# Kernel tuning notes

Hardware: AMD Instinct MI355X
Metric: run time of the kernel (lower is better)

The kernel has to match this reference:

```python
import jax, jax.numpy as jnp
import numpy as np

N = 100000        # nodes
E = 1600000       # edges (before self loops)
F_IN = 14         # Mutagenicity num_node_features
H = 64            # hidden_channels
C = 2             # Mutagenicity num_classes
G = 512           # graphs in batch
NEG_SLOPE = 0.2   # GATConv default leaky slope for attention logits


def setup_inputs() -> dict:
    key = jax.random.key(0)
    ks = jax.random.split(key, 40)
    inp = {
        "x": jax.random.normal(ks[0], (N, F_IN), jnp.float32),
        "edge_index": jax.random.randint(ks[1], (2, E), 0, N, dtype=jnp.int64),
        "batch": jnp.sort(jax.random.randint(ks[2], (N,), 0, G, dtype=jnp.int64)),
    }
    dims = [F_IN, H, H, H, H]
    ki = 3
    for l in range(5):
        fin = dims[l]
        s = 1.0 / np.sqrt(fin)
        inp[f"W{l}"] = jax.random.uniform(ks[ki], (fin, H), jnp.float32, -s, s); ki += 1
        inp[f"a_src{l}"] = jax.random.uniform(ks[ki], (H,), jnp.float32, -0.3, 0.3); ki += 1
        inp[f"a_dst{l}"] = jax.random.uniform(ks[ki], (H,), jnp.float32, -0.3, 0.3); ki += 1
        inp[f"b{l}"] = jnp.zeros((H,), jnp.float32)
    s = 1.0 / np.sqrt(H)
    inp["lin_W"] = jax.random.uniform(ks[ki], (H, C), jnp.float32, -s, s); ki += 1
    inp["lin_b"] = jnp.zeros((C,), jnp.float32)
    return inp


def _gat_layer(x, src, dst, W, a_s, a_d, b):
    # GATConv (heads=1): h = x W; e_ij = LeakyReLU(a_s.h_j + a_d.h_i);
    # alpha = softmax over incoming edges of node i; out_i = sum_j alpha_ij h_j + b
    h = x @ W                                   # [N, H]
    logit_s = h @ a_s                           # [N]
    logit_d = h @ a_d                           # [N]
    e = jax.nn.leaky_relu(logit_s[src] + logit_d[dst], NEG_SLOPE)  # [Etot]
    m = jax.ops.segment_max(e, dst, num_segments=N)
    m = jnp.where(jnp.isfinite(m), m, 0.0)      # empty segments -> 0 (none after self loops)
    ex = jnp.exp(e - m[dst])
    den = jax.ops.segment_sum(ex, dst, num_segments=N)
    alpha = ex / den[dst]                       # self loops guarantee den > 0
    out = jax.ops.segment_sum(alpha[:, None] * h[src], dst, num_segments=N)
    return out + b


def reference(x, edge_index, batch,
              W0, a_src0, a_dst0, b0,
              W1, a_src1, a_dst1, b1,
              W2, a_src2, a_dst2, b2,
              W3, a_src3, a_dst3, b3,
              W4, a_src4, a_dst4, b4,
              lin_W, lin_b):
    # add self loops once (GATConv default add_self_loops=True)
    loop = jnp.arange(N, dtype=edge_index.dtype)
    src = jnp.concatenate([edge_index[0], loop])
    dst = jnp.concatenate([edge_index[1], loop])

    h = x
    layers = [(W0, a_src0, a_dst0, b0), (W1, a_src1, a_dst1, b1),
              (W2, a_src2, a_dst2, b2), (W3, a_src3, a_dst3, b3),
              (W4, a_src4, a_dst4, b4)]
    for (W, a_s, a_d, b) in layers:
        h = jax.nn.elu(_gat_layer(h, src, dst, W, a_s, a_d, b))

    # global max pool over graphs
    g = jax.ops.segment_max(h, batch, num_segments=G)   # [G, H]
    g = jnp.where(jnp.isfinite(g), g, 0.0)
    return g @ lin_W + lin_b                             # [G, C]
```

## Files before the change

### kernel.cpp

```cpp
#include <hip/hip_runtime.h>
#include <hip/hip_fp16.h>
#include <math.h>

#define N_NODES 100000
#define H_DIM 64
#define G_GRAPHS 512
#define NEG_SLOPE 0.2f

#define BSHIFT 9
#define NBKT ((N_NODES + (1 << BSHIFT) - 1) >> BSHIFT)
#define CHUNK_E 4096

#define DEG_CAP 32

#define PK_SRC(v)  ((v) & 0x1FFFF)
#define PK_LD(v)   ((v) >> 17)

#if defined(__has_builtin)
#if __has_builtin(__builtin_amdgcn_fdot2)
#define HAS_FDOT2 1
#endif
#endif
#ifndef HAS_FDOT2
#define HAS_FDOT2 0
#endif

#if HAS_FDOT2
typedef _Float16 h2_t __attribute__((ext_vector_type(2)));
__device__ __forceinline__ h2_t as_h2(unsigned u) {
    h2_t r; __builtin_memcpy(&r, &u, 4); return r;
}
#endif


__global__ __launch_bounds__(256) void bucket_hist_kernel(const int* __restrict__ dst,
                                                          int* __restrict__ bcount, int E) {
    __shared__ int lh[NBKT];
    int t = threadIdx.x;
    for (int i = t; i < NBKT; i += 256) lh[i] = 0;
    __syncthreads();
    int base = blockIdx.x * CHUNK_E;
#pragma unroll
    for (int k = 0; k < 16; ++k) {
        int e = base + k * 256 + t;
        if (e < E) atomicAdd(&lh[dst[e] >> BSHIFT], 1);
    }
    __syncthreads();
    for (int i = t; i < NBKT; i += 256) {
        int c = lh[i];
        if (c) atomicAdd(&bcount[i], c);
    }
}

__global__ __launch_bounds__(256) void bucket_scan_kernel(const int* __restrict__ bcount,
                                                          int* __restrict__ bbase,
                                                          int* __restrict__ bfill,
                                                          int* __restrict__ off, int n) {
    __shared__ int sm[256];
    int t = threadIdx.x;
    sm[t] = (t < NBKT) ? bcount[t] : 0;
    __syncthreads();
    for (int d = 1; d < 256; d <<= 1) {
        int v = (t >= d) ? sm[t - d] : 0;
        __syncthreads();
        sm[t] += v;
        __syncthreads();
    }
    if (t < NBKT) {
        int ex = (t == 0) ? 0 : sm[t - 1];
        bbase[t] = ex;
        bfill[t] = ex;
    }
    if (t == 0) {
        bbase[NBKT] = sm[255];
        off[n] = sm[255];
    }
}

__global__ __launch_bounds__(256) void partition_kernel(const int* __restrict__ src,
                                                        const int* __restrict__ dst,
                                                        int* __restrict__ bfill,
                                                        int* __restrict__ ebuck, int E) {
    __shared__ int lh[NBKT];
    __shared__ int lbase[NBKT];
    int t = threadIdx.x;
    int base = blockIdx.x * CHUNK_E;
    for (int i = t; i < NBKT; i += 256) lh[i] = 0;
    __syncthreads();

    int pk[16], bk[16];
#pragma unroll
    for (int k = 0; k < 16; ++k) {
        int e = base + k * 256 + t;
        if (e < E) {
            int s = src[e];
            int d = dst[e];
            bk[k] = d >> BSHIFT;
            pk[k] = s | ((d & ((1 << BSHIFT) - 1)) << 17);
            atomicAdd(&lh[bk[k]], 1);
        } else {
            bk[k] = -1;
        }
    }
    __syncthreads();
    for (int i = t; i < NBKT; i += 256) {
        int c = lh[i];
        lbase[i] = c ? atomicAdd(&bfill[i], c) : 0;
        lh[i] = 0;
    }
    __syncthreads();
#pragma unroll
    for (int k = 0; k < 16; ++k) {
        if (bk[k] >= 0) {
            int r = atomicAdd(&lh[bk[k]], 1);
            ebuck[lbase[bk[k]] + r] = pk[k];
        }
    }
}

__global__ __launch_bounds__(256) void bucket_csr_kernel(const int* __restrict__ ebuck,
                                                         const int* __restrict__ bbase,
                                                         int* __restrict__ off,
                                                         int* __restrict__ esrc, int n) {
    __shared__ int cnt[512];
    __shared__ int loff[512];
    __shared__ int sm[256];
    int b = blockIdx.x;
    int t = threadIdx.x;
    int ebeg = bbase[b];
    int eend = bbase[b + 1];
    int nbeg = b << BSHIFT;
    int nloc = n - nbeg; if (nloc > 512) nloc = 512;

    cnt[t] = 0; cnt[t + 256] = 0;
    __syncthreads();
    for (int e = ebeg + t; e < eend; e += 256) {
        atomicAdd(&cnt[PK_LD(ebuck[e])], 1);
    }
    __syncthreads();
    int c0 = cnt[2 * t], c1 = cnt[2 * t + 1];
    sm[t] = c0 + c1;
    __syncthreads();
    for (int d = 1; d < 256; d <<= 1) {
        int v = (t >= d) ? sm[t - d] : 0;
        __syncthreads();
        sm[t] += v;
        __syncthreads();
    }
    int basep = (t == 0) ? 0 : sm[t - 1];
    loff[2 * t] = basep;
    loff[2 * t + 1] = basep + c0;
    cnt[2 * t] = 0; cnt[2 * t + 1] = 0;
    __syncthreads();
    for (int i = t; i < nloc; i += 256) off[nbeg + i] = ebeg + loff[i];
    for (int e = ebeg + t; e < eend; e += 256) {
        int v = ebuck[e];
        int d = PK_LD(v);
        int r = atomicAdd(&cnt[d], 1);
        esrc[ebeg + loff[d] + r] = PK_SRC(v);
    }
}

template <int FIN, int FINP, int XSTR>
__global__ __launch_bounds__(256) void gemm_tile_kernel(
        const float* __restrict__ act, const float* __restrict__ W,
        const float* __restrict__ a_s, const float* __restrict__ a_d,
        __half* __restrict__ h16g,
        float* __restrict__ ls, float* __restrict__ ld,
        int n) {
    __shared__ float sx[128 * XSTR];
    __shared__ float sw[FINP * 64];
    int t = threadIdx.x;
    int tb = blockIdx.x * 128;
    int nrow = n - tb; if (nrow > 128) nrow = 128;

    {
        const float4* Wv = (const float4*)W;
        float4* swv = (float4*)sw;
        for (int i = t; i < FINP * 16; i += 256) {
            int k = i >> 4;
            swv[i] = (k < FIN) ? Wv[i] : make_float4(0.0f, 0.0f, 0.0f, 0.0f);
        }
    }
    {
        int c = t & 15;
        for (int r = t >> 4; r < 128; r += 16) {
            float v = 0.0f;
            if (r < nrow && c < FIN) v = act[(size_t)(tb + r) * FIN + c];
            sx[r * XSTR + c] = v;
        }
    }
    __syncthreads();

    int f4 = t & 15;
    int ng = t >> 4;

    float4 acc[8];
#pragma unroll
    for (int i = 0; i < 8; ++i) acc[i] = make_float4(0.0f, 0.0f, 0.0f, 0.0f);

    for (int k4 = 0; k4 < FINP; k4 += 4) {
        float4 w0 = *(const float4*)(sw + (k4 + 0) * 64 + f4 * 4);
        float4 w1 = *(const float4*)(sw + (k4 + 1) * 64 + f4 * 4);
        float4 w2 = *(const float4*)(sw + (k4 + 2) * 64 + f4 * 4);
        float4 w3 = *(const float4*)(sw + (k4 + 3) * 64 + f4 * 4);
#pragma unroll
        for (int i = 0; i < 8; ++i) {
            float4 xv = *(const float4*)(sx + (ng + 16 * i) * XSTR + k4);
            acc[i].x = fmaf(xv.x, w0.x, acc[i].x);
            acc[i].y = fmaf(xv.x, w0.y, acc[i].y);
            acc[i].z = fmaf(xv.x, w0.z, acc[i].z);
            acc[i].w = fmaf(xv.x, w0.w, acc[i].w);
            acc[i].x = fmaf(xv.y, w1.x, acc[i].x);
            acc[i].y = fmaf(xv.y, w1.y, acc[i].y);
            acc[i].z = fmaf(xv.y, w1.z, acc[i].z);
            acc[i].w = fmaf(xv.y, w1.w, acc[i].w);
            acc[i].x = fmaf(xv.z, w2.x, acc[i].x);
            acc[i].y = fmaf(xv.z, w2.y, acc[i].y);
            acc[i].z = fmaf(xv.z, w2.z, acc[i].z);
            acc[i].w = fmaf(xv.z, w2.w, acc[i].w);
            acc[i].x = fmaf(xv.w, w3.x, acc[i].x);
            acc[i].y = fmaf(xv.w, w3.y, acc[i].y);
            acc[i].z = fmaf(xv.w, w3.z, acc[i].z);
            acc[i].w = fmaf(xv.w, w3.w, acc[i].w);
        }
    }

    float4 as4 = *(const float4*)(a_s + f4 * 4);
    float4 ad4 = *(const float4*)(a_d + f4 * 4);
#pragma unroll
    for (int i = 0; i < 8; ++i) {
        int r = ng + 16 * i;
        if (r < nrow) {
            int node = tb + r;
            __half2 plo = __floats2half2_rn(acc[i].x, acc[i].y);
            __half2 phi = __floats2half2_rn(acc[i].z, acc[i].w);
            uint2 pk;
            pk.x = *reinterpret_cast<unsigned*>(&plo);
            pk.y = *reinterpret_cast<unsigned*>(&phi);
            *reinterpret_cast<uint2*>(h16g + (size_t)node * 64 + f4 * 4) = pk;
            float vs = acc[i].x * as4.x + acc[i].y * as4.y +
                       acc[i].z * as4.z + acc[i].w * as4.w;
            float vd = acc[i].x * ad4.x + acc[i].y * ad4.y +
                       acc[i].z * ad4.z + acc[i].w * ad4.w;
            vs += __shfl_xor(vs, 1, 64); vd += __shfl_xor(vd, 1, 64);
            vs += __shfl_xor(vs, 2, 64); vd += __shfl_xor(vd, 2, 64);
            vs += __shfl_xor(vs, 4, 64); vd += __shfl_xor(vd, 4, 64);
            vs += __shfl_xor(vs, 8, 64); vd += __shfl_xor(vd, 8, 64);
            if (f4 == 0) { ls[node] = vs; ld[node] = vd; }
        }
    }
}

__global__ __launch_bounds__(256) void gat_gemm_kernel(
        const __half* __restrict__ h16_in, const float* __restrict__ ls_in,
        const float* __restrict__ ld_in, const int* __restrict__ off,
        const int* __restrict__ esrc, const float* __restrict__ bias,
        const float* __restrict__ Wn, const float* __restrict__ asn,
        const float* __restrict__ adn,
        __half* __restrict__ h16_out, float* __restrict__ ls_out,
        float* __restrict__ ld_out, int n) {
#if HAS_FDOT2
    __shared__ unsigned sw2[32 * 64];
#else
    __shared__ float sw[64 * 64];
#endif
    __shared__ int2 smq[16 * DEG_CAP];
    int t = threadIdx.x;
#if HAS_FDOT2
    for (int i = t; i < 32 * 64; i += 256) {
        int k2 = i >> 6, f = i & 63;
        float w0 = Wn[(2 * k2) * 64 + f];
        float w1 = Wn[(2 * k2 + 1) * 64 + f];
        __half2 wp = __floats2half2_rn(w0, w1);
        sw2[i] = *reinterpret_cast<unsigned*>(&wp);
    }
#else
    {
        const float4* Wv = (const float4*)Wn;
        float4* swv = (float4*)sw;
        for (int i = t; i < 64 * 16; i += 256) swv[i] = Wv[i];
    }
#endif
    __syncthreads();

    int fl = t & 15;
    int g = t >> 4;
    int node = blockIdx.x * 16 + g;
    if (node >= n) return;
    int2* sq = smq + g * DEG_CAP;
    int fl4 = fl * 4;
    int sk4 = 4 * g;

    int jb = off[node];
    int je = off[node + 1];
    int deg = je - jb;
    int degc = (deg < DEG_CAP) ? deg : DEG_CAP;
    float ldv = ld_in[node];
    float lself = ls_in[node];

    float mm = lself;
    for (int c = fl; c < degc; c += 16) {
        int s = esrc[jb + c];
        float v = ls_in[s];
        sq[(c + sk4) & (DEG_CAP - 1)] = make_int2(s, __float_as_int(v));
        mm = fmaxf(mm, v);
    }
    for (int c = degc + fl; c < deg; c += 16) {
        mm = fmaxf(mm, ls_in[esrc[jb + c]]);
    }
    mm = fmaxf(mm, __shfl_xor(mm, 8, 64));
    mm = fmaxf(mm, __shfl_xor(mm, 4, 64));
    mm = fmaxf(mm, __shfl_xor(mm, 2, 64));
    mm = fmaxf(mm, __shfl_xor(mm, 1, 64));
    float mraw = mm + ldv;
    float m = (mraw >= 0.0f) ? mraw : NEG_SLOPE * mraw;

    float denl = 0.0f;
    for (int c = fl; c < degc; c += 16) {
        int ci = (c + sk4) & (DEG_CAP - 1);
        float e = __int_as_float(sq[ci].y) + ldv;
        e = (e >= 0.0f) ? e : NEG_SLOPE * e;
        float p = __expf(e - m);
        sq[ci].y = __float_as_int(p);
        denl += p;
    }
    int degc4 = (degc + 3) & ~3;
    if (fl < degc4 - degc) sq[(degc + fl + sk4) & (DEG_CAP - 1)] = make_int2(node, 0);

    denl += __shfl_xor(denl, 8, 64);
    denl += __shfl_xor(denl, 4, 64);
    denl += __shfl_xor(denl, 2, 64);
    denl += __shfl_xor(denl, 1, 64);

    uint2 qs = *reinterpret_cast<const uint2*>(h16_in + (size_t)node * 64 + fl4);
    float2 sa = __half22float2(*reinterpret_cast<__half2*>(&qs.x));
    float2 sb = __half22float2(*reinterpret_cast<__half2*>(&qs.y));

    float4 acc = make_float4(0.0f, 0.0f, 0.0f, 0.0f);
    for (int c = 0; c < degc4; c += 4) {
        int2 e0 = sq[(c + 0 + sk4) & (DEG_CAP - 1)];
        int2 e1 = sq[(c + 1 + sk4) & (DEG_CAP - 1)];
        int2 e2 = sq[(c + 2 + sk4) & (DEG_CAP - 1)];
        int2 e3 = sq[(c + 3 + sk4) & (DEG_CAP - 1)];
        uint2 q0 = *reinterpret_cast<const uint2*>(h16_in + (size_t)e0.x * 64 + fl4);
        uint2 q1 = *reinterpret_cast<const uint2*>(h16_in + (size_t)e1.x * 64 + fl4);
        uint2 q2 = *reinterpret_cast<const uint2*>(h16_in + (size_t)e2.x * 64 + fl4);
        uint2 q3 = *reinterpret_cast<const uint2*>(h16_in + (size_t)e3.x * 64 + fl4);
        float p0 = __int_as_float(e0.y), p1 = __int_as_float(e1.y);
        float p2 = __int_as_float(e2.y), p3 = __int_as_float(e3.y);
        float2 a0 = __half22float2(*reinterpret_cast<__half2*>(&q0.x));
        float2 b0 = __half22float2(*reinterpret_cast<__half2*>(&q0.y));
        float2 a1 = __half22float2(*reinterpret_cast<__half2*>(&q1.x));
        float2 b1 = __half22float2(*reinterpret_cast<__half2*>(&q1.y));
        float2 a2 = __half22float2(*reinterpret_cast<__half2*>(&q2.x));
        float2 b2 = __half22float2(*reinterpret_cast<__half2*>(&q2.y));
        float2 a3 = __half22float2(*reinterpret_cast<__half2*>(&q3.x));
        float2 b3 = __half22float2(*reinterpret_cast<__half2*>(&q3.y));
        acc.x = fmaf(p0, a0.x, acc.x); acc.y = fmaf(p0, a0.y, acc.y);
        acc.z = fmaf(p0, b0.x, acc.z); acc.w = fmaf(p0, b0.y, acc.w);
        acc.x = fmaf(p1, a1.x, acc.x); acc.y = fmaf(p1, a1.y, acc.y);
        acc.z = fmaf(p1, b1.x, acc.z); acc.w = fmaf(p1, b1.y, acc.w);
        acc.x = fmaf(p2, a2.x, acc.x); acc.y = fmaf(p2, a2.y, acc.y);
        acc.z = fmaf(p2, b2.x, acc.z); acc.w = fmaf(p2, b2.y, acc.w);
        acc.x = fmaf(p3, a3.x, acc.x); acc.y = fmaf(p3, a3.y, acc.y);
        acc.z = fmaf(p3, b3.x, acc.z); acc.w = fmaf(p3, b3.y, acc.w);
    }

    float den_of = 0.0f;
    for (int j = jb + DEG_CAP; j < je; ++j) {
        int s = esrc[j];
        float e = ls_in[s] + ldv;
        e = (e >= 0.0f) ? e : NEG_SLOPE * e;
        float p = __expf(e - m);
        den_of += p;
        uint2 qv = *reinterpret_cast<const uint2*>(h16_in + (size_t)s * 64 + fl4);
        float2 va = __half22float2(*reinterpret_cast<__half2*>(&qv.x));
        float2 vb = __half22float2(*reinterpret_cast<__half2*>(&qv.y));
        acc.x = fmaf(p, va.x, acc.x);
        acc.y = fmaf(p, va.y, acc.y);
        acc.z = fmaf(p, vb.x, acc.z);
        acc.w = fmaf(p, vb.y, acc.w);
    }

    float e0s = lself + ldv;
    e0s = (e0s >= 0.0f) ? e0s : NEG_SLOPE * e0s;
    float p0s = __expf(e0s - m);
    float den = denl + den_of + p0s;
    acc.x = fmaf(p0s, sa.x, acc.x);
    acc.y = fmaf(p0s, sa.y, acc.y);
    acc.z = fmaf(p0s, sb.x, acc.z);
    acc.w = fmaf(p0s, sb.y, acc.w);

    const float4 b4 = *(const float4*)(bias + fl4);
    float inv = 1.0f / den;
    float4 o;
    o.x = acc.x * inv + b4.x;
    o.y = acc.y * inv + b4.y;
    o.z = acc.z * inv + b4.z;
    o.w = acc.w * inv + b4.w;
    o.x = (o.x > 0.0f) ? o.x : expm1f(o.x);
    o.y = (o.y > 0.0f) ? o.y : expm1f(o.y);
    o.z = (o.z > 0.0f) ? o.z : expm1f(o.z);
    o.w = (o.w > 0.0f) ? o.w : expm1f(o.w);

    float4 ha = make_float4(0.0f, 0.0f, 0.0f, 0.0f);
#if HAS_FDOT2
    {
        __half2 plo = __floats2half2_rn(o.x, o.y);
        __half2 phi = __floats2half2_rn(o.z, o.w);
        uint2 pk;
        pk.x = *reinterpret_cast<unsigned*>(&plo);
        pk.y = *reinterpret_cast<unsigned*>(&phi);
        uint2* so16 = (uint2*)sq;
        so16[(fl + g) & 15] = pk;
#pragma unroll
        for (int kk = 0; kk < 16; ++kk) {
            uint2 ov = so16[(kk + g) & 15];
            h2_t o01 = as_h2(ov.x);
            h2_t o23 = as_h2(ov.y);
            const uint4 wA = *reinterpret_cast<const uint4*>(sw2 + (2 * kk) * 64 + fl4);
            const uint4 wB = *reinterpret_cast<const uint4*>(sw2 + (2 * kk + 1) * 64 + fl4);
            ha.x = __builtin_amdgcn_fdot2(o01, as_h2(wA.x), ha.x, false);
            ha.y = __builtin_amdgcn_fdot2(o01, as_h2(wA.y), ha.y, false);
            ha.z = __builtin_amdgcn_fdot2(o01, as_h2(wA.z), ha.z, false);
            ha.w = __builtin_amdgcn_fdot2(o01, as_h2(wA.w), ha.w, false);
            ha.x = __builtin_amdgcn_fdot2(o23, as_h2(wB.x), ha.x, false);
            ha.y = __builtin_amdgcn_fdot2(o23, as_h2(wB.y), ha.y, false);
            ha.z = __builtin_amdgcn_fdot2(o23, as_h2(wB.z), ha.z, false);
            ha.w = __builtin_amdgcn_fdot2(o23, as_h2(wB.w), ha.w, false);
        }
    }
#else
    {
        float4* so = (float4*)sq;
        so[(fl + g) & 15] = o;
#pragma unroll
        for (int kk = 0; kk < 16; ++kk) {
            float4 ov = so[(kk + g) & 15];
            const float4 w0 = *(const float4*)(sw + (4 * kk + 0) * 64 + fl4);
            const float4 w1 = *(const float4*)(sw + (4 * kk + 1) * 64 + fl4);
            const float4 w2 = *(const float4*)(sw + (4 * kk + 2) * 64 + fl4);
            const float4 w3 = *(const float4*)(sw + (4 * kk + 3) * 64 + fl4);
            ha.x = fmaf(ov.x, w0.x, ha.x); ha.y = fmaf(ov.x, w0.y, ha.y);
            ha.z = fmaf(ov.x, w0.z, ha.z); ha.w = fmaf(ov.x, w0.w, ha.w);
            ha.x = fmaf(ov.y, w1.x, ha.x); ha.y = fmaf(ov.y, w1.y, ha.y);
            ha.z = fmaf(ov.y, w1.z, ha.z); ha.w = fmaf(ov.y, w1.w, ha.w);
            ha.x = fmaf(ov.z, w2.x, ha.x); ha.y = fmaf(ov.z, w2.y, ha.y);
            ha.z = fmaf(ov.z, w2.z, ha.z); ha.w = fmaf(ov.z, w2.w, ha.w);
            ha.x = fmaf(ov.w, w3.x, ha.x); ha.y = fmaf(ov.w, w3.y, ha.y);
            ha.z = fmaf(ov.w, w3.z, ha.z); ha.w = fmaf(ov.w, w3.w, ha.w);
        }
    }
#endif

    {
        __half2 plo = __floats2half2_rn(ha.x, ha.y);
        __half2 phi = __floats2half2_rn(ha.z, ha.w);
        uint2 pk;
        pk.x = *reinterpret_cast<unsigned*>(&plo);
        pk.y = *reinterpret_cast<unsigned*>(&phi);
        *reinterpret_cast<uint2*>(h16_out + (size_t)node * 64 + fl4) = pk;
    }
    float4 as4 = *(const float4*)(asn + fl4);
    float4 ad4 = *(const float4*)(adn + fl4);
    float vs = ha.x * as4.x + ha.y * as4.y + ha.z * as4.z + ha.w * as4.w;
    float vd = ha.x * ad4.x + ha.y * ad4.y + ha.z * ad4.z + ha.w * ad4.w;
    vs += __shfl_xor(vs, 1, 64); vd += __shfl_xor(vd, 1, 64);
    vs += __shfl_xor(vs, 2, 64); vd += __shfl_xor(vd, 2, 64);
    vs += __shfl_xor(vs, 4, 64); vd += __shfl_xor(vd, 4, 64);
    vs += __shfl_xor(vs, 8, 64); vd += __shfl_xor(vd, 8, 64);
    if (fl == 0) { ls_out[node] = vs; ld_out[node] = vd; }
}

__device__ __forceinline__ unsigned enc_f32(float f) {
    unsigned b = __float_as_uint(f);
    return (b & 0x80000000u) ? ~b : (b | 0x80000000u);
}

__global__ __launch_bounds__(256) void gat_final_pool_kernel(
        const __half* __restrict__ h16_in,
        const float* __restrict__ ls_in,
        const float* __restrict__ ld_in, const int* __restrict__ off,
        const int* __restrict__ esrc, const float* __restrict__ bias,
        const int* __restrict__ batch, unsigned* __restrict__ genc, int n) {
    __shared__ int2 smq[16 * DEG_CAP];
    __shared__ float sbo[16 * 64];
    __shared__ int sbb[16];
    int t = threadIdx.x;
    int fl = t & 15;
    int g = t >> 4;
    int node = blockIdx.x * 16 + g;
    bool active = node < n;
    int2* sq = smq + g * DEG_CAP;
    int fl4 = fl * 4;
    int sk4 = 4 * g;

    if (active) {
        int jb = off[node];
        int je = off[node + 1];
        int deg = je - jb;
        int degc = (deg < DEG_CAP) ? deg : DEG_CAP;
        float ldv = ld_in[node];
        float lself = ls_in[node];

        float mm = lself;
        for (int c = fl; c < degc; c += 16) {
            int s = esrc[jb + c];
            float v = ls_in[s];
            sq[(c + sk4) & (DEG_CAP - 1)] = make_int2(s, __float_as_int(v));
            mm = fmaxf(mm, v);
        }
        for (int c = degc + fl; c < deg; c += 16) {
            mm = fmaxf(mm, ls_in[esrc[jb + c]]);
        }
        mm = fmaxf(mm, __shfl_xor(mm, 8, 64));
        mm = fmaxf(mm, __shfl_xor(mm, 4, 64));
        mm = fmaxf(mm, __shfl_xor(mm, 2, 64));
        mm = fmaxf(mm, __shfl_xor(mm, 1, 64));
        float mraw = mm + ldv;
        float m = (mraw >= 0.0f) ? mraw : NEG_SLOPE * mraw;

        float denl = 0.0f;
        for (int c = fl; c < degc; c += 16) {
            int ci = (c + sk4) & (DEG_CAP - 1);
            float e = __int_as_float(sq[ci].y) + ldv;
            e = (e >= 0.0f) ? e : NEG_SLOPE * e;
            float p = __expf(e - m);
            sq[ci].y = __float_as_int(p);
            denl += p;
        }
        int degc4 = (degc + 3) & ~3;
        if (fl < degc4 - degc) sq[(degc + fl + sk4) & (DEG_CAP - 1)] = make_int2(node, 0);

        denl += __shfl_xor(denl, 8, 64);
        denl += __shfl_xor(denl, 4, 64);
        denl += __shfl_xor(denl, 2, 64);
        denl += __shfl_xor(denl, 1, 64);

        uint2 qs = *reinterpret_cast<const uint2*>(h16_in + (size_t)node * 64 + fl4);
        float2 sa = __half22float2(*reinterpret_cast<__half2*>(&qs.x));
        float2 sb = __half22float2(*reinterpret_cast<__half2*>(&qs.y));

        float4 acc = make_float4(0.0f, 0.0f, 0.0f, 0.0f);
        for (int c = 0; c < degc4; c += 4) {
            int2 e0 = sq[(c + 0 + sk4) & (DEG_CAP - 1)];
            int2 e1 = sq[(c + 1 + sk4) & (DEG_CAP - 1)];
            int2 e2 = sq[(c + 2 + sk4) & (DEG_CAP - 1)];
            int2 e3 = sq[(c + 3 + sk4) & (DEG_CAP - 1)];
            uint2 q0 = *reinterpret_cast<const uint2*>(h16_in + (size_t)e0.x * 64 + fl4);
            uint2 q1 = *reinterpret_cast<const uint2*>(h16_in + (size_t)e1.x * 64 + fl4);
            uint2 q2 = *reinterpret_cast<const uint2*>(h16_in + (size_t)e2.x * 64 + fl4);
            uint2 q3 = *reinterpret_cast<const uint2*>(h16_in + (size_t)e3.x * 64 + fl4);
            float p0 = __int_as_float(e0.y), p1 = __int_as_float(e1.y);
            float p2 = __int_as_float(e2.y), p3 = __int_as_float(e3.y);
            float2 a0 = __half22float2(*reinterpret_cast<__half2*>(&q0.x));
            float2 b0 = __half22float2(*reinterpret_cast<__half2*>(&q0.y));
            float2 a1 = __half22float2(*reinterpret_cast<__half2*>(&q1.x));
            float2 b1 = __half22float2(*reinterpret_cast<__half2*>(&q1.y));
            float2 a2 = __half22float2(*reinterpret_cast<__half2*>(&q2.x));
            float2 b2 = __half22float2(*reinterpret_cast<__half2*>(&q2.y));
            float2 a3 = __half22float2(*reinterpret_cast<__half2*>(&q3.x));
            float2 b3 = __half22float2(*reinterpret_cast<__half2*>(&q3.y));
            acc.x = fmaf(p0, a0.x, acc.x); acc.y = fmaf(p0, a0.y, acc.y);
            acc.z = fmaf(p0, b0.x, acc.z); acc.w = fmaf(p0, b0.y, acc.w);
            acc.x = fmaf(p1, a1.x, acc.x); acc.y = fmaf(p1, a1.y, acc.y);
            acc.z = fmaf(p1, b1.x, acc.z); acc.w = fmaf(p1, b1.y, acc.w);
            acc.x = fmaf(p2, a2.x, acc.x); acc.y = fmaf(p2, a2.y, acc.y);
            acc.z = fmaf(p2, b2.x, acc.z); acc.w = fmaf(p2, b2.y, acc.w);
            acc.x = fmaf(p3, a3.x, acc.x); acc.y = fmaf(p3, a3.y, acc.y);
            acc.z = fmaf(p3, b3.x, acc.z); acc.w = fmaf(p3, b3.y, acc.w);
        }

        float den_of = 0.0f;
        for (int j = jb + DEG_CAP; j < je; ++j) {
            int s = esrc[j];
            float e = ls_in[s] + ldv;
            e = (e >= 0.0f) ? e : NEG_SLOPE * e;
            float p = __expf(e - m);
            den_of += p;
            uint2 qv = *reinterpret_cast<const uint2*>(h16_in + (size_t)s * 64 + fl4);
            float2 va = __half22float2(*reinterpret_cast<__half2*>(&qv.x));
            float2 vb = __half22float2(*reinterpret_cast<__half2*>(&qv.y));
            acc.x = fmaf(p, va.x, acc.x);
            acc.y = fmaf(p, va.y, acc.y);
            acc.z = fmaf(p, vb.x, acc.z);
            acc.w = fmaf(p, vb.y, acc.w);
        }

        float e0s = lself + ldv;
        e0s = (e0s >= 0.0f) ? e0s : NEG_SLOPE * e0s;
        float p0s = __expf(e0s - m);
        float den = denl + den_of + p0s;
        acc.x = fmaf(p0s, sa.x, acc.x);
        acc.y = fmaf(p0s, sa.y, acc.y);
        acc.z = fmaf(p0s, sb.x, acc.z);
        acc.w = fmaf(p0s, sb.y, acc.w);

        const float4 b4 = *(const float4*)(bias + fl4);
        float inv = 1.0f / den;
        float4 o;
        o.x = acc.x * inv + b4.x;
        o.y = acc.y * inv + b4.y;
        o.z = acc.z * inv + b4.z;
        o.w = acc.w * inv + b4.w;
        o.x = (o.x > 0.0f) ? o.x : expm1f(o.x);
        o.y = (o.y > 0.0f) ? o.y : expm1f(o.y);
        o.z = (o.z > 0.0f) ? o.z : expm1f(o.z);
        o.w = (o.w > 0.0f) ? o.w : expm1f(o.w);

        *(float4*)(sbo + g * 64 + fl4) = o;
        if (fl == 0) sbb[g] = batch[node];
    }
    __syncthreads();

    if (t < 64) {
        int nval = n - blockIdx.x * 16;
        if (nval > 16) nval = 16;
        if (nval > 0) {
            int cur = sbb[0];
            float rm = -1e38f;
            for (int gg = 0; gg < nval; ++gg) {
                int b = sbb[gg];
                if (b != cur) {
                    atomicMax(&genc[cur * 64 + t], enc_f32(rm));
                    cur = b;
                    rm = -1e38f;
                }
                rm = fmaxf(rm, sbo[gg * 64 + t]);
            }
            atomicMax(&genc[cur * 64 + t], enc_f32(rm));
        }
    }
}

__global__ __launch_bounds__(64) void final_kernel(const unsigned* __restrict__ genc,
                                                   const float* __restrict__ linW,
                                                   const float* __restrict__ linb,
                                                   float* __restrict__ out) {
    int g = blockIdx.x;
    int lane = threadIdx.x;
    unsigned u = genc[g * 64 + lane];
    float v;
    if (u == 0u) {
        v = 0.0f;
    } else {
        unsigned b = (u & 0x80000000u) ? (u ^ 0x80000000u) : ~u;
        v = __uint_as_float(b);
    }
    float c0 = v * linW[lane * 2 + 0];
    float c1 = v * linW[lane * 2 + 1];
#pragma unroll
    for (int d = 32; d >= 1; d >>= 1) {
        c0 += __shfl_xor(c0, d, 64);
        c1 += __shfl_xor(c1, d, 64);
    }
    if (lane == 0) {
        out[g * 2 + 0] = c0 + linb[0];
        out[g * 2 + 1] = c1 + linb[1];
    }
}

static inline size_t align_up(size_t v, size_t a) { return (v + a - 1) & ~(a - 1); }

extern "C" void kernel_launch(void* const* d_in, const int* in_sizes, int n_in,
                              void* d_out, int out_size, void* d_ws, size_t ws_size,
                              hipStream_t stream) {
    const float* x          = (const float*)d_in[0];
    const int*   edge_index = (const int*)d_in[1];
    const int*   batch      = (const int*)d_in[2];
    const float* W[5];
    const float* a_s[5];
    const float* a_d[5];
    const float* bias[5];
    for (int l = 0; l < 5; ++l) {
        W[l]    = (const float*)d_in[3 + 4 * l + 0];
        a_s[l]  = (const float*)d_in[3 + 4 * l + 1];
        a_d[l]  = (const float*)d_in[3 + 4 * l + 2];
        bias[l] = (const float*)d_in[3 + 4 * l + 3];
    }
    const float* linW = (const float*)d_in[23];
    const float* linb = (const float*)d_in[24];
    float* out = (float*)d_out;

    const int N = N_NODES;
    const int E = in_sizes[1] / 2;
    const int* srcp = edge_index;
    const int* dstp = edge_index + E;

    char* p = (char*)d_ws;
    int* bcount = (int*)p;        p += align_up((size_t)NBKT * 4, 256);
    int* bbase  = (int*)p;        p += align_up((size_t)(NBKT + 1) * 4, 256);
    int* bfill  = (int*)p;        p += align_up((size_t)NBKT * 4, 256);
    int* off    = (int*)p;        p += align_up((size_t)(N + 1) * 4, 256);
    int* esrc   = (int*)p;        p += align_up((size_t)E * 4, 256);
    float* lsA  = (float*)p;      p += align_up((size_t)N * 4, 256);
    float* ldA  = (float*)p;      p += align_up((size_t)N * 4, 256);
    float* lsB  = (float*)p;      p += align_up((size_t)N * 4, 256);
    float* ldB  = (float*)p;      p += align_up((size_t)N * 4, 256);
    __half* h16A = (__half*)p;    p += align_up((size_t)N * 64 * 2, 256);
    __half* h16B = (__half*)p;    p += align_up((size_t)N * 64 * 2, 256);
    unsigned* genc = (unsigned*)p; p += align_up((size_t)G_GRAPHS * 64 * 4, 256);

    int* ebuck = (int*)h16B;

    hipMemsetAsync(bcount, 0, (size_t)NBKT * 4, stream);
    hipMemsetAsync(genc, 0, (size_t)G_GRAPHS * 64 * 4, stream);

    int pb2 = (E + CHUNK_E - 1) / CHUNK_E;
    bucket_hist_kernel<<<pb2, 256, 0, stream>>>(dstp, bcount, E);
    bucket_scan_kernel<<<1, 256, 0, stream>>>(bcount, bbase, bfill, off, N);
    partition_kernel<<<pb2, 256, 0, stream>>>(srcp, dstp, bfill, ebuck, E);
    bucket_csr_kernel<<<NBKT, 256, 0, stream>>>(ebuck, bbase, off, esrc, N);

    int nb = (N + 15) / 16;
    int gt = (N + 127) / 128;

    gemm_tile_kernel<14, 16, 20><<<gt, 256, 0, stream>>>(
        x, W[0], a_s[0], a_d[0], h16A, lsA, ldA, N);
    gat_gemm_kernel<<<nb, 256, 0, stream>>>(
        h16A, lsA, ldA, off, esrc, bias[0], W[1], a_s[1], a_d[1],
        h16B, lsB, ldB, N);
    gat_gemm_kernel<<<nb, 256, 0, stream>>>(
        h16B, lsB, ldB, off, esrc, bias[1], W[2], a_s[2], a_d[2],
        h16A, lsA, ldA, N);
    gat_gemm_kernel<<<nb, 256, 0, stream>>>(
        h16A, lsA, ldA, off, esrc, bias[2], W[3], a_s[3], a_d[3],
        h16B, lsB, ldB, N);
    gat_gemm_kernel<<<nb, 256, 0, stream>>>(
        h16B, lsB, ldB, off, esrc, bias[3], W[4], a_s[4], a_d[4],
        h16A, lsA, ldA, N);
    gat_final_pool_kernel<<<nb, 256, 0, stream>>>(
        h16A, lsA, ldA, off, esrc, bias[4], batch, genc, N);

    final_kernel<<<G_GRAPHS, 64, 0, stream>>>(genc, linW, linb, out);
}
```

Before: 401.4 us.

## Process nodes in degree-sorted order to balance work in GAT layers

Adds a counting sort of nodes by in-degree (histogram, scan, scatter) that builds a permutation. The four middle GAT layer kernels then map each 16-lane group to a node through this permutation, so that nodes sharing a wavefront have similar degree. This aims to cut intra-wavefront divergence and load imbalance in the edge loops. In exchange it adds three small kernels and an extra indirection, and output writes and neighbour reads lose their natural node-order locality.

```diff
diff --git a/kernel.cpp b/kernel.cpp
--- a/kernel.cpp
+++ b/kernel.cpp
@@ -12,6 +12,7 @@
 #define CHUNK_E 4096
 
 #define DEG_CAP 32
+#define DBINS 512
 
 #define PK_SRC(v)  ((v) & 0x1FFFF)
 #define PK_LD(v)   ((v) >> 17)
@@ -158,6 +159,81 @@
         int d = PK_LD(v);
         int r = atomicAdd(&cnt[d], 1);
         esrc[ebeg + loff[d] + r] = PK_SRC(v);
+    }
+}
+
+__global__ __launch_bounds__(256) void deg_hist_kernel(const int* __restrict__ off,
+                                                       int* __restrict__ dcount, int n) {
+    __shared__ int lh[DBINS];
+    int t = threadIdx.x;
+    lh[t] = 0; lh[t + 256] = 0;
+    __syncthreads();
+    int base = blockIdx.x * 2048;
+#pragma unroll
+    for (int k = 0; k < 8; ++k) {
+        int i = base + k * 256 + t;
+        if (i < n) {
+            int d = off[i + 1] - off[i];
+            if (d > DBINS - 1) d = DBINS - 1;
+            atomicAdd(&lh[d], 1);
+        }
+    }
+    __syncthreads();
+    int c0 = lh[t];       if (c0) atomicAdd(&dcount[t], c0);
+    int c1 = lh[t + 256]; if (c1) atomicAdd(&dcount[t + 256], c1);
+}
+
+__global__ __launch_bounds__(256) void deg_scan_kernel(const int* __restrict__ dcount,
+                                                       int* __restrict__ dfill) {
+    __shared__ int sm[256];
+    int t = threadIdx.x;
+    int c0 = dcount[2 * t], c1 = dcount[2 * t + 1];
+    sm[t] = c0 + c1;
+    __syncthreads();
+    for (int d = 1; d < 256; d <<= 1) {
+        int v = (t >= d) ? sm[t - d] : 0;
+        __syncthreads();
+        sm[t] += v;
+        __syncthreads();
+    }
+    int basep = (t == 0) ? 0 : sm[t - 1];
+    dfill[2 * t] = basep;
+    dfill[2 * t + 1] = basep + c0;
+}
+
+__global__ __launch_bounds__(256) void deg_scatter_kernel(const int* __restrict__ off,
+                                                          int* __restrict__ dfill,
+                                                          int* __restrict__ perm, int n) {
+    __shared__ int lh[DBINS];
+    __shared__ int lbase[DBINS];
+    int t = threadIdx.x;
+    for (int i = t; i < DBINS; i += 256) lh[i] = 0;
+    __syncthreads();
+    int base = blockIdx.x * 2048;
+    int d[8];
+#pragma unroll
+    for (int k = 0; k < 8; ++k) {
+        int i = base + k * 256 + t;
+        if (i < n) {
+            int dd = off[i + 1] - off[i];
+            if (dd > DBINS - 1) dd = DBINS - 1;
+            d[k] = dd;
+            atomicAdd(&lh[dd], 1);
+        } else d[k] = -1;
+    }
+    __syncthreads();
+    for (int i = t; i < DBINS; i += 256) {
+        int c = lh[i];
+        lbase[i] = c ? atomicAdd(&dfill[i], c) : 0;
+        lh[i] = 0;
+    }
+    __syncthreads();
+#pragma unroll
+    for (int k = 0; k < 8; ++k) {
+        if (d[k] >= 0) {
+            int r = atomicAdd(&lh[d[k]], 1);
+            perm[lbase[d[k]] + r] = base + k * 256 + t;
+        }
     }
 }
 
@@ -255,7 +331,8 @@
 __global__ __launch_bounds__(256) void gat_gemm_kernel(
         const __half* __restrict__ h16_in, const float* __restrict__ ls_in,
         const float* __restrict__ ld_in, const int* __restrict__ off,
-        const int* __restrict__ esrc, const float* __restrict__ bias,
+        const int* __restrict__ esrc, const int* __restrict__ perm,
+        const float* __restrict__ bias,
         const float* __restrict__ Wn, const float* __restrict__ asn,
         const float* __restrict__ adn,
         __half* __restrict__ h16_out, float* __restrict__ ls_out,
@@ -286,8 +363,9 @@
 
     int fl = t & 15;
     int g = t >> 4;
-    int node = blockIdx.x * 16 + g;
-    if (node >= n) return;
+    int idx = blockIdx.x * 16 + g;
+    if (idx >= n) return;
+    int node = perm[idx];
     int2* sq = smq + g * DEG_CAP;
     int fl4 = fl * 4;
     int sk4 = 4 * g;
@@ -690,10 +768,13 @@
 
     char* p = (char*)d_ws;
     int* bcount = (int*)p;        p += align_up((size_t)NBKT * 4, 256);
+    int* dcount = (int*)p;        p += align_up((size_t)DBINS * 4, 256);
     int* bbase  = (int*)p;        p += align_up((size_t)(NBKT + 1) * 4, 256);
     int* bfill  = (int*)p;        p += align_up((size_t)NBKT * 4, 256);
+    int* dfill  = (int*)p;        p += align_up((size_t)DBINS * 4, 256);
     int* off    = (int*)p;        p += align_up((size_t)(N + 1) * 4, 256);
     int* esrc   = (int*)p;        p += align_up((size_t)E * 4, 256);
+    int* perm   = (int*)p;        p += align_up((size_t)N * 4, 256);
     float* lsA  = (float*)p;      p += align_up((size_t)N * 4, 256);
     float* ldA  = (float*)p;      p += align_up((size_t)N * 4, 256);
     float* lsB  = (float*)p;      p += align_up((size_t)N * 4, 256);
@@ -704,7 +785,7 @@
 
     int* ebuck = (int*)h16B;
 
-    hipMemsetAsync(bcount, 0, (size_t)NBKT * 4, stream);
+    hipMemsetAsync(bcount, 0, align_up((size_t)NBKT * 4, 256) + (size_t)DBINS * 4, stream);
     hipMemsetAsync(genc, 0, (size_t)G_GRAPHS * 64 * 4, stream);
 
     int pb2 = (E + CHUNK_E - 1) / CHUNK_E;
@@ -713,22 +794,27 @@
     partition_kernel<<<pb2, 256, 0, stream>>>(srcp, dstp, bfill, ebuck, E);
     bucket_csr_kernel<<<NBKT, 256, 0, stream>>>(ebuck, bbase, off, esrc, N);
 
+    int db = (N + 2047) / 2048;
+    deg_hist_kernel<<<db, 256, 0, stream>>>(off, dcount, N);
+    deg_scan_kernel<<<1, 256, 0, stream>>>(dcount, dfill);
+    deg_scatter_kernel<<<db, 256, 0, stream>>>(off, dfill, perm, N);
+
     int nb = (N + 15) / 16;
     int gt = (N + 127) / 128;
 
     gemm_tile_kernel<14, 16, 20><<<gt, 256, 0, stream>>>(
         x, W[0], a_s[0], a_d[0], h16A, lsA, ldA, N);
     gat_gemm_kernel<<<nb, 256, 0, stream>>>(
-        h16A, lsA, ldA, off, esrc, bias[0], W[1], a_s[1], a_d[1],
+        h16A, lsA, ldA, off, esrc, perm, bias[0], W[1], a_s[1], a_d[1],
         h16B, lsB, ldB, N);
     gat_gemm_kernel<<<nb, 256, 0, stream>>>(
-        h16B, lsB, ldB, off, esrc, bias[1], W[2], a_s[2], a_d[2],
+        h16B, lsB, ldB, off, esrc, perm, bias[1], W[2], a_s[2], a_d[2],
         h16A, lsA, ldA, N);
     gat_gemm_kernel<<<nb, 256, 0, stream>>>(
-        h16A, lsA, ldA, off, esrc, bias[2], W[3], a_s[3], a_d[3],
+        h16A, lsA, ldA, off, esrc, perm, bias[2], W[3], a_s[3], a_d[3],
         h16B, lsB, ldB, N);
     gat_gemm_kernel<<<nb, 256, 0, stream>>>(
-        h16B, lsB, ldB, off, esrc, bias[3], W[4], a_s[4], a_d[4],
+        h16B, lsB, ldB, off, esrc, perm, bias[3], W[4], a_s[4], a_d[4],
         h16A, lsA, ldA, N);
     gat_final_pool_kernel<<<nb, 256, 0, stream>>>(
         h16A, lsA, ldA, off, esrc, bias[4], batch, genc, N);
```

Result: no change. 408.1 us (+1.7%).
